# Kernel optimization log

Measured on AMD Instinct MI355X. Metric: run time of the kernel, lower is better.

Reference implementation:

```python
import jax, jax.numpy as jnp
import numpy as np

SMALL_NUM = 0.015
B, R, F, H, A = 262144, 3, 4, 16, 18  # batch, rules, features-per-rule, hidden, action_dim


def setup_inputs() -> dict:
    key = jax.random.key(0)
    ks = jax.random.split(key, 10)
    s = jax.random.normal(ks[0], (B, F), dtype=jnp.float32)
    # membership-network params, stacked over (rule, feature); xavier-uniform-ish scales
    W1 = jax.random.uniform(ks[1], (R, F, H), minval=-1.0, maxval=1.0) * np.sqrt(6.0 / (1 + H))
    b1 = jnp.zeros((R, F, H), jnp.float32)
    W2 = jax.random.uniform(ks[2], (R, F, H, H), minval=-1.0, maxval=1.0) * np.sqrt(6.0 / (2 * H))
    b2 = jnp.zeros((R, F, H), jnp.float32)
    W3 = jax.random.uniform(ks[3], (R, F, H), minval=-1.0, maxval=1.0) * np.sqrt(6.0 / (H + 1))
    b3 = jnp.zeros((R, F), jnp.float32)
    # p_select init per Rule.__init__: column 0 = 0, column 1 = 10
    p_select = jnp.concatenate([jnp.zeros((R, F, 1)), jnp.full((R, F, 1), 10.0)], axis=-1).astype(jnp.float32)
    leaves_params = jax.random.normal(ks[4], (4, A), dtype=jnp.float32)
    # Gumbel(0,1) noise, drawn once (the torch module samples inside forward)
    U = jax.random.uniform(ks[5], (R, F, 2), minval=1e-6, maxval=1.0)
    gumbel_noise = -jnp.log(-jnp.log(U + 1e-20) + 1e-20)
    return {"s": s, "W1": W1, "b1": b1, "W2": W2, "b2": b2, "W3": W3, "b3": b3,
            "p_select": p_select, "leaves_params": leaves_params, "gumbel_noise": gumbel_noise}


def reference(s, W1, b1, W2, b2, W3, b3, p_select, leaves_params, gumbel_noise):
    lrelu = lambda x: jnp.where(x > 0, x, 0.01 * x)  # F.leaky_relu default slope
    # all 12 tiny MLPs (3 rules x 4 features) vectorized; input is the scalar feature s[:, f]
    h1 = lrelu(jnp.einsum('bf,rfh->brfh', s, W1) + b1)            # [B,R,F,H]
    h2 = lrelu(jnp.einsum('brfh,rfho->brfo', h1, W2) + b2)        # [B,R,F,H]
    m = jax.nn.sigmoid(jnp.einsum('brfh,rfh->brf', h2, W3) + b3)  # [B,R,F] membership
    m = jnp.maximum(m, SMALL_NUM)  # torch.where(m < SMALL, SMALL, m)
    # hard gumbel-softmax over last dim (torch dim=1 of a [F,2] tensor), straight-through
    y_soft = jax.nn.softmax(p_select + gumbel_noise, axis=-1)     # [R,F,2]
    y_hard = (y_soft == y_soft.max(-1, keepdims=True)).astype(y_soft.dtype)
    gs = jax.lax.stop_gradient(y_hard - y_soft) + y_soft
    gs1 = gs[..., 1]                                              # [R,F]
    soft_weight = gs1[None] / m                                   # [B,R,F]
    X_exp = jnp.exp(soft_weight * 0.1)
    cond = gs1.sum(-1) > SMALL_NUM                                # [R] per-rule masked softmax
    X_exp = jnp.where(cond[None, :, None], X_exp * gs1[None], X_exp)
    soft = X_exp / X_exp.sum(-1, keepdims=True)
    strength = (m * soft * gs1[None]).sum(-1)                     # [B,R]
    strength = jnp.where(jnp.isnan(strength), 0.0, strength)
    r0, r1, r2 = strength[:, 0:1], strength[:, 1:2], strength[:, 2:3]
    path_p = jnp.concatenate([r0 * r1, r0 * (1 - r1), (1 - r0) * r2, (1 - r0) * (1 - r2)], axis=1)  # [B,4]
    idx = jnp.argmax(path_p, axis=1)
    leaves_distribution = jax.nn.softmax(leaves_params, axis=1)   # [4,A]
    return leaves_distribution[idx]                               # [B,A]
```

## Files before the change

### kernel.cpp

```cpp
#include <hip/hip_runtime.h>
#include <math.h>

#define BTOT 262144
#define R 3
#define F 4
#define H 16
#define A 18
#define SMALL_NUM_F 0.015f
#define MARGIN_TAU 1e-4f

#define WS_FLAG   0
#define WS_COUNT  1
#define WS_KP     4
#define WS_KM     20
#define WS_G      40
#define WS_COND   52
#define WS_LEAVES 56
#define WS_B3     128
#define WS_HDR_FLOATS 192
#define WS_HDR_BYTES  768

__global__ __launch_bounds__(256) void ftc_setup(
    const float* __restrict__ W1, const float* __restrict__ b1,
    const float* __restrict__ W2, const float* __restrict__ b2,
    const float* __restrict__ W3, const float* __restrict__ b3,
    const float* __restrict__ p_select, const float* __restrict__ gumbel,
    const float* __restrict__ leaves,
    float* __restrict__ ws)
{
    __shared__ int nz;
    __shared__ float sh_g[R * F];
    const int tid = threadIdx.x;
    if (tid == 0) nz = 0;
    __syncthreads();
    if (tid < R * F * H) {
        if (b1[tid] != 0.0f) atomicOr(&nz, 1);
        if (b2[tid] != 0.0f) atomicOr(&nz, 1);
    }

    if (tid < R * F) {
        const int rf = tid;
        float l0 = p_select[rf * 2 + 0] + gumbel[rf * 2 + 0];
        float l1 = p_select[rf * 2 + 1] + gumbel[rf * 2 + 1];
        float mx = fmaxf(l0, l1);
        float e0 = expf(l0 - mx), e1 = expf(l1 - mx);
        float den = e0 + e1;
        float y0 = e0 / den, y1 = e1 / den;
        float ym = fmaxf(y0, y1);
        float g = (y1 == ym) ? 1.0f : 0.0f;
        sh_g[rf] = g;
        ws[WS_G + rf] = g;
        ws[WS_B3 + rf] = b3[rf];
    }
    if (tid < 4) {
        float mx = leaves[tid * A];
        for (int a = 1; a < A; ++a) mx = fmaxf(mx, leaves[tid * A + a]);
        float e[A];
        float sum = 0.f;
        for (int a = 0; a < A; ++a) { e[a] = expf(leaves[tid * A + a] - mx); sum += e[a]; }
        for (int a = 0; a < A; ++a) ws[WS_LEAVES + tid * A + a] = e[a] / sum;
    }
    if (tid < R * F) {
        const int rf = tid;
        double Kp = 0.0, Km = 0.0;
        for (int o = 0; o < H; ++o) {
            double Pp = 0.0, Pm = 0.0;
            for (int h = 0; h < H; ++h) {
                const double w1 = (double)W1[rf * H + h];
                const double w2 = (double)W2[rf * H * H + h * H + o];
                Pp += w1 * ((w1 > 0.0) ? 1.0 : 0.01) * w2;
                Pm += w1 * ((w1 < 0.0) ? 1.0 : 0.01) * w2;
            }
            const double w3 = (double)W3[rf * H + o];
            Kp += Pp * ((Pp > 0.0) ? 1.0 : 0.01) * w3;
            Km += Pm * ((Pm < 0.0) ? 1.0 : 0.01) * w3;
        }
        ws[WS_KP + rf] = (float)Kp;
        ws[WS_KM + rf] = (float)Km;
    }
    __syncthreads();
    if (tid == 0) {
        ((int*)ws)[WS_FLAG]  = (nz == 0) ? 1 : 0;
        ((int*)ws)[WS_COUNT] = 0;
    }
    if (tid < R) {
        float ssum = sh_g[tid * F + 0] + sh_g[tid * F + 1] + sh_g[tid * F + 2] + sh_g[tid * F + 3];
        ws[WS_COND + tid] = (ssum > SMALL_NUM_F) ? 1.0f : 0.0f;
    }
}

__device__ __forceinline__ void compute_m_exact(
    const float sf[F],
    const float* __restrict__ W1, const float* __restrict__ b1,
    const float* __restrict__ W2, const float* __restrict__ b2,
    const float* __restrict__ W3, const float* __restrict__ b3,
    float m[R][F])
{
#pragma unroll
    for (int r = 0; r < R; ++r) {
#pragma unroll
        for (int f = 0; f < F; ++f) {
            const int rf = r * F + f;
            const float* w1  = W1 + rf * H;
            const float* bb1 = b1 + rf * H;
            const float* w2  = W2 + rf * H * H;
            const float* bb2 = b2 + rf * H;
            const float* w3  = W3 + rf * H;
            float h1[H];
#pragma unroll
            for (int h = 0; h < H; ++h) {
                float v = fmaf(sf[f], w1[h], bb1[h]);
                h1[h] = fmaxf(v, 0.01f * v);
            }
            float acc[H];
#pragma unroll
            for (int o = 0; o < H; ++o) acc[o] = bb2[o];
#pragma unroll
            for (int h = 0; h < H; ++h) {
                const float hv = h1[h];
#pragma unroll
                for (int o = 0; o < H; ++o)
                    acc[o] = fmaf(hv, w2[h * H + o], acc[o]);
            }
            float dot = b3[rf];
#pragma unroll
            for (int o = 0; o < H; ++o) {
                float v = fmaxf(acc[o], 0.01f * acc[o]);
                dot = fmaf(v, w3[o], dot);
            }
            float mm = 1.0f / (1.0f + expf(-dot));
            m[r][f] = fmaxf(mm, SMALL_NUM_F);
        }
    }
}

__device__ __forceinline__ void compute_strength_exact(
    const float m[R][F], const float g[R][F], const float cond[R], float st[R])
{
#pragma unroll
    for (int r = 0; r < R; ++r) {
        const bool c = cond[r] != 0.0f;
        float X[F];
        float ssum = 0.f;
#pragma unroll
        for (int f = 0; f < F; ++f) {
            float gv = g[r][f];
            float xw = expf(0.1f * (gv / m[r][f]));
            if (c) xw *= gv;
            X[f] = xw;
            ssum += xw;
        }
        float sv = 0.f;
#pragma unroll
        for (int f = 0; f < F; ++f)
            sv += m[r][f] * (X[f] / ssum) * g[r][f];
        st[r] = isnan(sv) ? 0.0f : sv;
    }
}

__device__ __forceinline__ int path_argmax(const float st[R]) {
    const float r0 = st[0], r1 = st[1], r2 = st[2];
    const float p0 = r0 * r1;
    const float p1 = r0 * (1.0f - r1);
    const float p2 = (1.0f - r0) * r2;
    const float p3 = (1.0f - r0) * (1.0f - r2);
    int idx = 0;
    float best = p0;
    if (p1 > best) { best = p1; idx = 1; }
    if (p2 > best) { best = p2; idx = 2; }
    if (p3 > best) { best = p3; idx = 3; }
    return idx;
}

template<bool USE_LIST>
__global__ __launch_bounds__(256) void ftc_main(
    const float* __restrict__ s,
    const float* __restrict__ W1, const float* __restrict__ b1,
    const float* __restrict__ W2, const float* __restrict__ b2,
    const float* __restrict__ W3, const float* __restrict__ b3,
    float* __restrict__ ws,
    unsigned int* __restrict__ list,
    float* __restrict__ out)
{
    __shared__ float sh_hdr[WS_HDR_FLOATS];
    __shared__ unsigned char sh_idx[256];

    const int tid = threadIdx.x;
    if (tid < WS_HDR_FLOATS) sh_hdr[tid] = ws[tid];
    __syncthreads();

    const int flag = (int)__float_as_uint(sh_hdr[WS_FLAG]);

    const int b = blockIdx.x * 256 + tid;
    const float4 sv = *reinterpret_cast<const float4*>(s + (size_t)b * F);
    const float sf[F] = {sv.x, sv.y, sv.z, sv.w};

    float st[R];
    bool need_exact = true;

    if (flag) {
#pragma unroll
        for (int r = 0; r < R; ++r) {
            const bool c = sh_hdr[WS_COND + r] != 0.0f;
            float num = 0.f, den = 0.f;
#pragma unroll
            for (int f = 0; f < F; ++f) {
                const int rf = r * F + f;
                const float k = (sf[f] > 0.0f) ? sh_hdr[WS_KP + rf] : sh_hdr[WS_KM + rf];
                const float dot = fmaf(sf[f], k, sh_hdr[WS_B3 + rf]);
                const float inv_m = fminf(1.0f + __expf(-dot), 1.0f / SMALL_NUM_F);
                const float mm = __builtin_amdgcn_rcpf(inv_m);
                const float g = sh_hdr[WS_G + rf];
                float xw = __expf(0.1f * g * inv_m);
                if (c) xw *= g;
                num = fmaf(mm * xw, g, num);
                den += xw;
            }
            st[r] = num * __builtin_amdgcn_rcpf(den);
        }
        const float r0 = st[0], r1 = st[1], r2 = st[2];
        const float p0 = r0 * r1;
        const float p1 = r0 * (1.0f - r1);
        const float p2 = (1.0f - r0) * r2;
        const float p3 = (1.0f - r0) * (1.0f - r2);
        const float a = fmaxf(p0, p1), bb = fminf(p0, p1);
        const float c2 = fmaxf(p2, p3), d = fminf(p2, p3);
        const float best = fmaxf(a, c2);
        const float second = fmaxf(fminf(a, c2), (a >= c2) ? bb : d);
        need_exact = !((best - second) > MARGIN_TAU);
    }

    if constexpr (USE_LIST) {
        if (flag) {
            if (need_exact) {
                unsigned int pos = atomicAdd((unsigned int*)ws + WS_COUNT, 1u);
                list[pos] = (unsigned int)b;
            }
        } else {
            float g[R][F], cond[R], m[R][F];
#pragma unroll
            for (int r = 0; r < R; ++r) {
                cond[r] = sh_hdr[WS_COND + r];
#pragma unroll
                for (int f = 0; f < F; ++f) g[r][f] = sh_hdr[WS_G + r * F + f];
            }
            compute_m_exact(sf, W1, b1, W2, b2, W3, b3, m);
            compute_strength_exact(m, g, cond, st);
        }
    } else {
        if (need_exact) {
            float g[R][F], cond[R], m[R][F];
#pragma unroll
            for (int r = 0; r < R; ++r) {
                cond[r] = sh_hdr[WS_COND + r];
#pragma unroll
                for (int f = 0; f < F; ++f) g[r][f] = sh_hdr[WS_G + r * F + f];
            }
            compute_m_exact(sf, W1, b1, W2, b2, W3, b3, m);
            compute_strength_exact(m, g, cond, st);
        }
    }

    sh_idx[tid] = (unsigned char)path_argmax(st);
    __syncthreads();

    float* outb = out + (size_t)blockIdx.x * (256 * A);
    for (int i = tid; i < 256 * A; i += 256) {
        int bl = i / A;
        int a  = i - bl * A;
        outb[i] = sh_hdr[WS_LEAVES + (int)sh_idx[bl] * A + a];
    }
}

#define W2S 260
__global__ __launch_bounds__(256) void ftc_cleanup(
    const float* __restrict__ s,
    const float* __restrict__ W1, const float* __restrict__ b1,
    const float* __restrict__ W2, const float* __restrict__ b2,
    const float* __restrict__ W3, const float* __restrict__ b3,
    const float* __restrict__ ws,
    const unsigned int* __restrict__ list,
    float* __restrict__ out)
{
    const int count = ((const int*)ws)[WS_COUNT];
    if ((int)blockIdx.x * 16 >= count) return;

    __shared__ float shW1[12 * 17], shB1[12 * 17], shB2[12 * 17], shW3[12 * 17];
    __shared__ float shW2[12 * W2S];
    __shared__ float shB3[12], shG[12], shCond[3], shLeaves[4 * A];

    const int tid = threadIdx.x;
    for (int i = tid; i < 192; i += 256) {
        const int rf = i >> 4, k = i & 15;
        shW1[rf * 17 + k] = W1[i];
        shB1[rf * 17 + k] = b1[i];
        shB2[rf * 17 + k] = b2[i];
        shW3[rf * 17 + k] = W3[i];
    }
    for (int i = tid; i < 3072; i += 256) {
        const int rf = i >> 8, k = i & 255;
        shW2[rf * W2S + k] = W2[i];
    }
    if (tid < 12) { shB3[tid] = ws[WS_B3 + tid]; shG[tid] = ws[WS_G + tid]; }
    if (tid < 3)  shCond[tid] = ws[WS_COND + tid];
    if (tid < 4 * A) shLeaves[tid] = ws[WS_LEAVES + tid];
    __syncthreads();

    const int l = tid & 15;
    const int g0 = blockIdx.x * 16 + (tid >> 4);

    for (int i = g0; i < count; i += gridDim.x * 16) {
        const int e = (int)list[i];
        float mval = 0.f;
        if (l < 12) {
            const int rf = l;
            const int f = rf & 3;
            const float sfv = s[(size_t)e * F + f];
            float h1[H];
#pragma unroll
            for (int h = 0; h < H; ++h) {
                float v = fmaf(sfv, shW1[rf * 17 + h], shB1[rf * 17 + h]);
                h1[h] = fmaxf(v, 0.01f * v);
            }
            float acc[H];
#pragma unroll
            for (int o = 0; o < H; ++o) acc[o] = shB2[rf * 17 + o];
#pragma unroll
            for (int h = 0; h < H; ++h) {
                const float hv = h1[h];
#pragma unroll
                for (int c4 = 0; c4 < 4; ++c4) {
                    const float4 w2v = *reinterpret_cast<const float4*>(
                        &shW2[rf * W2S + h * 16 + c4 * 4]);
                    acc[c4 * 4 + 0] = fmaf(hv, w2v.x, acc[c4 * 4 + 0]);
                    acc[c4 * 4 + 1] = fmaf(hv, w2v.y, acc[c4 * 4 + 1]);
                    acc[c4 * 4 + 2] = fmaf(hv, w2v.z, acc[c4 * 4 + 2]);
                    acc[c4 * 4 + 3] = fmaf(hv, w2v.w, acc[c4 * 4 + 3]);
                }
            }
            float dot = shB3[rf];
#pragma unroll
            for (int o = 0; o < H; ++o) {
                float v = fmaxf(acc[o], 0.01f * acc[o]);
                dot = fmaf(v, shW3[rf * 17 + o], dot);
            }
            float mm = 1.0f / (1.0f + expf(-dot));
            mval = fmaxf(mm, SMALL_NUM_F);
        }
        float m[R][F], g[R][F], cond[R], st[R];
#pragma unroll
        for (int j = 0; j < 12; ++j) {
            const float mv = __shfl(mval, j, 16);
            m[j >> 2][j & 3] = mv;
        }
#pragma unroll
        for (int r = 0; r < R; ++r) {
            cond[r] = shCond[r];
#pragma unroll
            for (int f = 0; f < F; ++f) g[r][f] = shG[r * F + f];
        }
        compute_strength_exact(m, g, cond, st);
        const int idx = path_argmax(st);
        for (int a = l; a < A; a += 16)
            out[(size_t)e * A + a] = shLeaves[idx * A + a];
    }
}

extern "C" void kernel_launch(void* const* d_in, const int* in_sizes, int n_in,
                              void* d_out, int out_size, void* d_ws, size_t ws_size,
                              hipStream_t stream) {
    const float* s  = (const float*)d_in[0];
    const float* W1 = (const float*)d_in[1];
    const float* b1 = (const float*)d_in[2];
    const float* W2 = (const float*)d_in[3];
    const float* b2 = (const float*)d_in[4];
    const float* W3 = (const float*)d_in[5];
    const float* b3 = (const float*)d_in[6];
    const float* ps = (const float*)d_in[7];
    const float* lv = (const float*)d_in[8];
    const float* gn = (const float*)d_in[9];
    float* ws  = (float*)d_ws;
    float* out = (float*)d_out;
    unsigned int* list = (unsigned int*)((char*)d_ws + WS_HDR_BYTES);
    const bool use_list = ws_size >= (size_t)WS_HDR_BYTES + sizeof(unsigned int) * (size_t)BTOT;

    hipLaunchKernelGGL(ftc_setup, dim3(1), dim3(256), 0, stream,
                       W1, b1, W2, b2, W3, b3, ps, gn, lv, ws);
    if (use_list) {
        hipLaunchKernelGGL((ftc_main<true>), dim3(BTOT / 256), dim3(256), 0, stream,
                           s, W1, b1, W2, b2, W3, b3, ws, list, out);
        hipLaunchKernelGGL(ftc_cleanup, dim3(512), dim3(256), 0, stream,
                           s, W1, b1, W2, b2, W3, b3, ws, list, out);
    } else {
        hipLaunchKernelGGL((ftc_main<false>), dim3(BTOT / 256), dim3(256), 0, stream,
                           s, W1, b1, W2, b2, W3, b3, ws, (unsigned int*)nullptr, out);
    }
}
```

Baseline: 41.96 us.

## Fold setup kernel into main blocks and vectorize leaf output stores

```diff
diff --git a/kernel.cpp b/kernel.cpp
--- a/kernel.cpp
+++ b/kernel.cpp
@@ -9,85 +9,8 @@
 #define SMALL_NUM_F 0.015f
 #define MARGIN_TAU 1e-4f
 
-#define WS_FLAG   0
-#define WS_COUNT  1
-#define WS_KP     4
-#define WS_KM     20
-#define WS_G      40
-#define WS_COND   52
-#define WS_LEAVES 56
-#define WS_B3     128
-#define WS_HDR_FLOATS 192
-#define WS_HDR_BYTES  768
-
-__global__ __launch_bounds__(256) void ftc_setup(
-    const float* __restrict__ W1, const float* __restrict__ b1,
-    const float* __restrict__ W2, const float* __restrict__ b2,
-    const float* __restrict__ W3, const float* __restrict__ b3,
-    const float* __restrict__ p_select, const float* __restrict__ gumbel,
-    const float* __restrict__ leaves,
-    float* __restrict__ ws)
-{
-    __shared__ int nz;
-    __shared__ float sh_g[R * F];
-    const int tid = threadIdx.x;
-    if (tid == 0) nz = 0;
-    __syncthreads();
-    if (tid < R * F * H) {
-        if (b1[tid] != 0.0f) atomicOr(&nz, 1);
-        if (b2[tid] != 0.0f) atomicOr(&nz, 1);
-    }
-
-    if (tid < R * F) {
-        const int rf = tid;
-        float l0 = p_select[rf * 2 + 0] + gumbel[rf * 2 + 0];
-        float l1 = p_select[rf * 2 + 1] + gumbel[rf * 2 + 1];
-        float mx = fmaxf(l0, l1);
-        float e0 = expf(l0 - mx), e1 = expf(l1 - mx);
-        float den = e0 + e1;
-        float y0 = e0 / den, y1 = e1 / den;
-        float ym = fmaxf(y0, y1);
-        float g = (y1 == ym) ? 1.0f : 0.0f;
-        sh_g[rf] = g;
-        ws[WS_G + rf] = g;
-        ws[WS_B3 + rf] = b3[rf];
-    }
-    if (tid < 4) {
-        float mx = leaves[tid * A];
-        for (int a = 1; a < A; ++a) mx = fmaxf(mx, leaves[tid * A + a]);
-        float e[A];
-        float sum = 0.f;
-        for (int a = 0; a < A; ++a) { e[a] = expf(leaves[tid * A + a] - mx); sum += e[a]; }
-        for (int a = 0; a < A; ++a) ws[WS_LEAVES + tid * A + a] = e[a] / sum;
-    }
-    if (tid < R * F) {
-        const int rf = tid;
-        double Kp = 0.0, Km = 0.0;
-        for (int o = 0; o < H; ++o) {
-            double Pp = 0.0, Pm = 0.0;
-            for (int h = 0; h < H; ++h) {
-                const double w1 = (double)W1[rf * H + h];
-                const double w2 = (double)W2[rf * H * H + h * H + o];
-                Pp += w1 * ((w1 > 0.0) ? 1.0 : 0.01) * w2;
-                Pm += w1 * ((w1 < 0.0) ? 1.0 : 0.01) * w2;
-            }
-            const double w3 = (double)W3[rf * H + o];
-            Kp += Pp * ((Pp > 0.0) ? 1.0 : 0.01) * w3;
-            Km += Pm * ((Pm < 0.0) ? 1.0 : 0.01) * w3;
-        }
-        ws[WS_KP + rf] = (float)Kp;
-        ws[WS_KM + rf] = (float)Km;
-    }
-    __syncthreads();
-    if (tid == 0) {
-        ((int*)ws)[WS_FLAG]  = (nz == 0) ? 1 : 0;
-        ((int*)ws)[WS_COUNT] = 0;
-    }
-    if (tid < R) {
-        float ssum = sh_g[tid * F + 0] + sh_g[tid * F + 1] + sh_g[tid * F + 2] + sh_g[tid * F + 3];
-        ws[WS_COND + tid] = (ssum > SMALL_NUM_F) ? 1.0f : 0.0f;
-    }
-}
+#define WS_COUNT 0
+#define WS_HDR_BYTES 768
 
 __device__ __forceinline__ void compute_m_exact(
     const float sf[F],
@@ -172,45 +95,109 @@
     return idx;
 }
 
+__device__ __forceinline__ void block_compute_gumbel_leaves(
+    const float* __restrict__ p_select, const float* __restrict__ gumbel,
+    const float* __restrict__ leaves, const float* __restrict__ b3,
+    int tid, float* shG, float* shB3, float* shCond, float2 (*shL2)[9])
+{
+    if (tid < R * F) {
+        const int rf = tid;
+        float l0 = p_select[rf * 2 + 0] + gumbel[rf * 2 + 0];
+        float l1 = p_select[rf * 2 + 1] + gumbel[rf * 2 + 1];
+        float mx = fmaxf(l0, l1);
+        float e0 = expf(l0 - mx), e1 = expf(l1 - mx);
+        float den = e0 + e1;
+        float y0 = e0 / den, y1 = e1 / den;
+        float ym = fmaxf(y0, y1);
+        shG[rf] = (y1 == ym) ? 1.0f : 0.0f;
+        shB3[rf] = b3[rf];
+    }
+    if (tid < 4) {
+        float mx = leaves[tid * A];
+        for (int a = 1; a < A; ++a) mx = fmaxf(mx, leaves[tid * A + a]);
+        float e[A];
+        float sum = 0.f;
+        for (int a = 0; a < A; ++a) { e[a] = expf(leaves[tid * A + a] - mx); sum += e[a]; }
+        for (int a = 0; a < 9; ++a)
+            shL2[tid][a] = make_float2(e[2 * a] / sum, e[2 * a + 1] / sum);
+    }
+    __syncthreads();
+    if (tid < R) {
+        float ssum = shG[tid * F + 0] + shG[tid * F + 1] + shG[tid * F + 2] + shG[tid * F + 3];
+        shCond[tid] = (ssum > SMALL_NUM_F) ? 1.0f : 0.0f;
+    }
+}
+
 template<bool USE_LIST>
 __global__ __launch_bounds__(256) void ftc_main(
     const float* __restrict__ s,
     const float* __restrict__ W1, const float* __restrict__ b1,
     const float* __restrict__ W2, const float* __restrict__ b2,
     const float* __restrict__ W3, const float* __restrict__ b3,
-    float* __restrict__ ws,
+    const float* __restrict__ p_select, const float* __restrict__ leaves,
+    const float* __restrict__ gumbel,
+    unsigned int* __restrict__ ws_count,
     unsigned int* __restrict__ list,
     float* __restrict__ out)
 {
-    __shared__ float sh_hdr[WS_HDR_FLOATS];
+    __shared__ double shPp[R * F * H], shPm[R * F * H];
+    __shared__ float shKP[R * F], shKM[R * F], shG[R * F], shB3[R * F];
+    __shared__ float shCond[R];
+    __shared__ float2 shL2[4][9];
+    __shared__ int shNZ;
     __shared__ unsigned char sh_idx[256];
 
     const int tid = threadIdx.x;
-    if (tid < WS_HDR_FLOATS) sh_hdr[tid] = ws[tid];
-    __syncthreads();
-
-    const int flag = (int)__float_as_uint(sh_hdr[WS_FLAG]);
+    if (tid == 0) shNZ = 0;
+    __syncthreads();
+
+    if (tid < R * F * H) {
+        if (b1[tid] != 0.0f || b2[tid] != 0.0f) atomicOr(&shNZ, 1);
+        const int rf = tid >> 4, o = tid & 15;
+        double Pp = 0.0, Pm = 0.0;
+        for (int h = 0; h < H; ++h) {
+            const double w1 = (double)W1[rf * H + h];
+            const double w2 = (double)W2[rf * H * H + h * H + o];
+            Pp += w1 * ((w1 > 0.0) ? 1.0 : 0.01) * w2;
+            Pm += w1 * ((w1 < 0.0) ? 1.0 : 0.01) * w2;
+        }
+        const double w3 = (double)W3[rf * H + o];
+        shPp[tid] = Pp * ((Pp > 0.0) ? 1.0 : 0.01) * w3;
+        shPm[tid] = Pm * ((Pm < 0.0) ? 1.0 : 0.01) * w3;
+    }
+    block_compute_gumbel_leaves(p_select, gumbel, leaves, b3, tid,
+                                shG, shB3, shCond, shL2);
+    __syncthreads();
+    if (tid < R * F) {
+        double Kp = 0.0, Km = 0.0;
+        for (int o = 0; o < H; ++o) { Kp += shPp[tid * H + o]; Km += shPm[tid * H + o]; }
+        shKP[tid] = (float)Kp;
+        shKM[tid] = (float)Km;
+    }
+    __syncthreads();
+
+    const int flag = (shNZ == 0) ? 1 : 0;
 
     const int b = blockIdx.x * 256 + tid;
     const float4 sv = *reinterpret_cast<const float4*>(s + (size_t)b * F);
     const float sf[F] = {sv.x, sv.y, sv.z, sv.w};
 
-    float st[R];
+    float st[R] = {0.f, 0.f, 0.f};
     bool need_exact = true;
 
     if (flag) {
 #pragma unroll
         for (int r = 0; r < R; ++r) {
-            const bool c = sh_hdr[WS_COND + r] != 0.0f;
+            const bool c = shCond[r] != 0.0f;
             float num = 0.f, den = 0.f;
 #pragma unroll
             for (int f = 0; f < F; ++f) {
                 const int rf = r * F + f;
-                const float k = (sf[f] > 0.0f) ? sh_hdr[WS_KP + rf] : sh_hdr[WS_KM + rf];
-                const float dot = fmaf(sf[f], k, sh_hdr[WS_B3 + rf]);
+                const float k = (sf[f] > 0.0f) ? shKP[rf] : shKM[rf];
+                const float dot = fmaf(sf[f], k, shB3[rf]);
                 const float inv_m = fminf(1.0f + __expf(-dot), 1.0f / SMALL_NUM_F);
                 const float mm = __builtin_amdgcn_rcpf(inv_m);
-                const float g = sh_hdr[WS_G + rf];
+                const float g = shG[rf];
                 float xw = __expf(0.1f * g * inv_m);
                 if (c) xw *= g;
                 num = fmaf(mm * xw, g, num);
@@ -231,30 +218,18 @@
     }
 
     if constexpr (USE_LIST) {
-        if (flag) {
-            if (need_exact) {
-                unsigned int pos = atomicAdd((unsigned int*)ws + WS_COUNT, 1u);
-                list[pos] = (unsigned int)b;
-            }
-        } else {
-            float g[R][F], cond[R], m[R][F];
-#pragma unroll
-            for (int r = 0; r < R; ++r) {
-                cond[r] = sh_hdr[WS_COND + r];
-#pragma unroll
-                for (int f = 0; f < F; ++f) g[r][f] = sh_hdr[WS_G + r * F + f];
-            }
-            compute_m_exact(sf, W1, b1, W2, b2, W3, b3, m);
-            compute_strength_exact(m, g, cond, st);
+        if (need_exact) {
+            unsigned int pos = atomicAdd(ws_count, 1u);
+            list[pos] = (unsigned int)b;
         }
     } else {
         if (need_exact) {
             float g[R][F], cond[R], m[R][F];
 #pragma unroll
             for (int r = 0; r < R; ++r) {
-                cond[r] = sh_hdr[WS_COND + r];
-#pragma unroll
-                for (int f = 0; f < F; ++f) g[r][f] = sh_hdr[WS_G + r * F + f];
+                cond[r] = shCond[r];
+#pragma unroll
+                for (int f = 0; f < F; ++f) g[r][f] = shG[r * F + f];
             }
             compute_m_exact(sf, W1, b1, W2, b2, W3, b3, m);
             compute_strength_exact(m, g, cond, st);
@@ -264,11 +239,11 @@
     sh_idx[tid] = (unsigned char)path_argmax(st);
     __syncthreads();
 
-    float* outb = out + (size_t)blockIdx.x * (256 * A);
-    for (int i = tid; i < 256 * A; i += 256) {
-        int bl = i / A;
-        int a  = i - bl * A;
-        outb[i] = sh_hdr[WS_LEAVES + (int)sh_idx[bl] * A + a];
+    float2* outb = reinterpret_cast<float2*>(out + (size_t)blockIdx.x * (256 * A));
+    for (int j = tid; j < 256 * (A / 2); j += 256) {
+        const int bl = j / 9;
+        const int off = j - bl * 9;
+        outb[j] = shL2[sh_idx[bl]][off];
     }
 }
 
@@ -278,16 +253,19 @@
     const float* __restrict__ W1, const float* __restrict__ b1,
     const float* __restrict__ W2, const float* __restrict__ b2,
     const float* __restrict__ W3, const float* __restrict__ b3,
-    const float* __restrict__ ws,
+    const float* __restrict__ p_select, const float* __restrict__ leaves,
+    const float* __restrict__ gumbel,
+    const unsigned int* __restrict__ ws_count,
     const unsigned int* __restrict__ list,
     float* __restrict__ out)
 {
-    const int count = ((const int*)ws)[WS_COUNT];
+    const int count = (int)*ws_count;
     if ((int)blockIdx.x * 16 >= count) return;
 
     __shared__ float shW1[12 * 17], shB1[12 * 17], shB2[12 * 17], shW3[12 * 17];
     __shared__ float shW2[12 * W2S];
-    __shared__ float shB3[12], shG[12], shCond[3], shLeaves[4 * A];
+    __shared__ float shG[R * F], shB3[R * F], shCond[R];
+    __shared__ float2 shL2[4][9];
 
     const int tid = threadIdx.x;
     for (int i = tid; i < 192; i += 256) {
@@ -301,9 +279,8 @@
         const int rf = i >> 8, k = i & 255;
         shW2[rf * W2S + k] = W2[i];
     }
-    if (tid < 12) { shB3[tid] = ws[WS_B3 + tid]; shG[tid] = ws[WS_G + tid]; }
-    if (tid < 3)  shCond[tid] = ws[WS_COND + tid];
-    if (tid < 4 * A) shLeaves[tid] = ws[WS_LEAVES + tid];
+    block_compute_gumbel_leaves(p_select, gumbel, leaves, b3, tid,
+                                shG, shB3, shCond, shL2);
     __syncthreads();
 
     const int l = tid & 15;
@@ -361,8 +338,9 @@
         }
         compute_strength_exact(m, g, cond, st);
         const int idx = path_argmax(st);
+        const float* lrow = reinterpret_cast<const float*>(&shL2[idx][0]);
         for (int a = l; a < A; a += 16)
-            out[(size_t)e * A + a] = shLeaves[idx * A + a];
+            out[(size_t)e * A + a] = lrow[a];
     }
 }
 
@@ -379,20 +357,20 @@
     const float* ps = (const float*)d_in[7];
     const float* lv = (const float*)d_in[8];
     const float* gn = (const float*)d_in[9];
-    float* ws  = (float*)d_ws;
     float* out = (float*)d_out;
+    unsigned int* ws_count = (unsigned int*)d_ws;
     unsigned int* list = (unsigned int*)((char*)d_ws + WS_HDR_BYTES);
     const bool use_list = ws_size >= (size_t)WS_HDR_BYTES + sizeof(unsigned int) * (size_t)BTOT;
 
-    hipLaunchKernelGGL(ftc_setup, dim3(1), dim3(256), 0, stream,
-                       W1, b1, W2, b2, W3, b3, ps, gn, lv, ws);
     if (use_list) {
+        hipMemsetAsync(d_ws, 0, WS_HDR_BYTES, stream);
         hipLaunchKernelGGL((ftc_main<true>), dim3(BTOT / 256), dim3(256), 0, stream,
-                           s, W1, b1, W2, b2, W3, b3, ws, list, out);
-        hipLaunchKernelGGL(ftc_cleanup, dim3(512), dim3(256), 0, stream,
-                           s, W1, b1, W2, b2, W3, b3, ws, list, out);
+                           s, W1, b1, W2, b2, W3, b3, ps, lv, gn, ws_count, list, out);
+        hipLaunchKernelGGL(ftc_cleanup, dim3(1024), dim3(256), 0, stream,
+                           s, W1, b1, W2, b2, W3, b3, ps, lv, gn, ws_count, list, out);
     } else {
         hipLaunchKernelGGL((ftc_main<false>), dim3(BTOT / 256), dim3(256), 0, stream,
-                           s, W1, b1, W2, b2, W3, b3, ws, (unsigned int*)nullptr, out);
-    }
-}
+                           s, W1, b1, W2, b2, W3, b3, ps, lv, gn,
+                           (unsigned int*)nullptr, (unsigned int*)nullptr, out);
+    }
+}
```

Result: no change. 42.72 us (+1.8%).
